# Performance work log

Measured on AMD Instinct MI355X. Metric: run time of the kernel, lower is better.

Reference implementation:

```python
import jax, jax.numpy as jnp
from jax import lax
import numpy as np

EPS_DENOM = 1e-5
EPS_NCC = 1e-5
HIGH = 0.5  # IntensityNormalization(high=0.5): min-max rescale of weights to [0, high]


def _box_conv(v, kernel):
    # Dense ones-kernel 3D box filter, VALID padding, stride 1 (NCDHW / OIDHW).
    return lax.conv_general_dilated(
        v, kernel, window_strides=(1, 1, 1), padding='VALID',
        dimension_numbers=('NCDHW', 'OIDHW', 'NCDHW'))


def setup_inputs() -> dict:
    key = jax.random.key(0)
    k1, k2 = jax.random.split(key)
    shape = (2, 1, 160, 192, 160)
    y_pred = jax.random.normal(k1, shape, dtype=jnp.float32)
    y_true = jax.random.normal(k2, shape, dtype=jnp.float32)
    kernel = jnp.ones((1, 1, 7, 7, 7), dtype=jnp.float32)
    return {"y_pred": y_pred, "y_true": y_true, "kernel": kernel}


def reference(y_pred, y_true, kernel):
    nw = kernel.sum()  # = 343 for a 7^3 ones kernel
    x, y = y_pred, y_true
    sum_x = _box_conv(x, kernel)
    sum_y = _box_conv(y, kernel)
    sum_x2 = _box_conv(x * x, kernel)
    sum_y2 = _box_conv(y * y, kernel)
    sum_xy = _box_conv(x * y, kernel)

    mean_x = sum_x / nw
    mean_y = sum_y / nw
    num = sum_xy + mean_x * mean_y * nw - mean_x * sum_y - mean_y * sum_x
    denom_0 = mean_x * mean_x * nw + sum_x2 - 2.0 * mean_x * sum_x
    denom_1 = mean_y * mean_y * nw + sum_y2 - 2.0 * mean_y * sum_y
    denom = denom_0 * denom_1

    valid = denom > EPS_DENOM
    safe_denom = jnp.where(valid, denom, 1.0)
    ncc = jnp.where(valid, num / jnp.sqrt(safe_denom), 0.0)
    invalid = (ncc < -1.0 - EPS_NCC) | (ncc > 1.0 + EPS_NCC)
    ncc = jnp.where(invalid, 0.0, ncc)
    all_valid = valid & ~invalid

    # Intensity normalization of weights: min-max rescale of local variance sum
    # over the valid voxels to [0, HIGH], then normalize to sum to 1.
    v = 0.5 * (denom_0 + denom_1)
    vmin = jnp.min(jnp.where(all_valid, v, jnp.inf))
    vmax = jnp.max(jnp.where(all_valid, v, -jnp.inf))
    w = jnp.where(all_valid, (v - vmin) / (vmax - vmin + 1e-12) * HIGH, 0.0)
    w = w / w.sum()

    return 1.0 - jnp.sum(jnp.where(all_valid, ncc, 0.0) * w)
```

## Files before the change

### kernel.cpp

```cpp
#include <hip/hip_runtime.h>
#include <math.h>

#define NN 2
#define DD 160
#define HH 192
#define WW 160
#define DO 154
#define HO 186
#define WO 154

#define NWO 3
#define HOT 8
#define NHO 24
#define ZCH 8
#define ZOC 20
#define NB (NWO * NHO * NN * ZCH)

#define LDS_SYNC() do { __builtin_amdgcn_s_waitcnt(0xC07F); __builtin_amdgcn_s_barrier(); } while (0)

__device__ __forceinline__ float block_sum(float v, float* sm) {
  int tid = threadIdx.x;
  sm[tid] = v;
  __syncthreads();
#pragma unroll
  for (int off = 128; off > 0; off >>= 1) {
    if (tid < off) sm[tid] += sm[tid + off];
    __syncthreads();
  }
  float r = sm[0];
  __syncthreads();
  return r;
}

__device__ __forceinline__ float block_min(float v, float* sm) {
  int tid = threadIdx.x;
  sm[tid] = v;
  __syncthreads();
#pragma unroll
  for (int off = 128; off > 0; off >>= 1) {
    if (tid < off) sm[tid] = fminf(sm[tid], sm[tid + off]);
    __syncthreads();
  }
  float r = sm[0];
  __syncthreads();
  return r;
}

__device__ __forceinline__ float wave_sum(float v) {
  v += __shfl_xor(v, 32); v += __shfl_xor(v, 16); v += __shfl_xor(v, 8);
  v += __shfl_xor(v, 4);  v += __shfl_xor(v, 2);  v += __shfl_xor(v, 1);
  return v;
}

__device__ __forceinline__ float wave_min(float v) {
  v = fminf(v, __shfl_xor(v, 32)); v = fminf(v, __shfl_xor(v, 16));
  v = fminf(v, __shfl_xor(v, 8));  v = fminf(v, __shfl_xor(v, 4));
  v = fminf(v, __shfl_xor(v, 2));  v = fminf(v, __shfl_xor(v, 1));
  return v;
}

#define SLIDE7(V, M) do { \
  float s0 = ((V[0]+V[1])+(V[2]+V[3])) + ((V[4]+V[5])+V[6]); \
  float s1 = s0 - V[0] + V[7]; \
  float s2 = s1 - V[1] + V[8]; \
  float s3 = s2 - V[2] + V[9]; \
  float s4 = s3 - V[3] + V[10]; \
  float s5 = s4 - V[4] + V[11]; \
  float s6 = s5 - V[5] + V[12]; \
  float s7 = s6 - V[6] + V[13]; \
  *(float4*)&R[M][0][rA][c4] = make_float4(s0, s1, s2, s3); \
  *(float4*)&R[M][1][rA][c4] = make_float4(s4, s5, s6, s7); \
} while (0)

__global__ __launch_bounds__(256, 3) void ncc_fused(const float* __restrict__ X,
                                                    const float* __restrict__ Y,
                                                    float* __restrict__ part) {
  __shared__ __align__(16) float R[5][2][14][64];
  __shared__ __align__(16) float Mh[5][HOT][64];
  __shared__ float red[4][5];

  const int tid = threadIdx.x;
  const int tx = tid & 63, ty = tid >> 6;
  const int wo0 = blockIdx.x * 64;
  const int ho0 = blockIdx.y * HOT;
  const int n   = blockIdx.z >> 3;
  const int ck  = blockIdx.z & 7;
  const int z0  = ck * ZOC;
  const int zout = min(ZOC, DO - z0);
  const int nslice = zout + 6;

  const int wo = wo0 + tx;
  const bool act0 = (wo < WO) && (ho0 + ty < HO);
  const bool act1 = (wo < WO) && (ho0 + ty + 4 < HO);

  const size_t slice = (size_t)HH * WW;
  const float* Xn = X + (size_t)n * DD * slice;
  const float* Yn = Y + (size_t)n * DD * slice;
  const float inv_nw = 1.0f / 343.0f;
  const float LO = -1.0f - 1e-5f, HI = 1.0f + 1e-5f;

  const int pA  = tid;
  const bool hasA = (pA < 112);
  const int rA  = pA >> 3;
  const int c8  = (pA & 7) << 3;
  const int c4  = (pA & 7) << 2;
  const int hA  = ho0 + rA;
  const int baseW = wo0 + c8;
  const bool okA  = hasA && (hA < HH) && (baseW < WO);
  const bool tail = okA && (baseW + 14 > WW);
  const float* XrowA = Xn + (size_t)hA * WW + baseW;
  const float* YrowA = Yn + (size_t)hA * WW + baseW;

  float4 lx0={0,0,0,0}, lx1={0,0,0,0}, lx2={0,0,0,0};
  float4 ly0={0,0,0,0}, ly1={0,0,0,0}, ly2={0,0,0,0};
  float2 lx3={0,0}, ly3={0,0};

  auto loadA = [&](int s_in) {
    if (okA) {
      const float* xp = XrowA + (size_t)(z0 + s_in) * slice;
      const float* yp = YrowA + (size_t)(z0 + s_in) * slice;
      lx0 = *(const float4*)xp;       lx1 = *(const float4*)(xp + 4);
      ly0 = *(const float4*)yp;       ly1 = *(const float4*)(yp + 4);
      if (!tail) {
        lx2 = *(const float4*)(xp + 8); lx3 = *(const float2*)(xp + 12);
        ly2 = *(const float4*)(yp + 8); ly3 = *(const float2*)(yp + 12);
      } else {
        lx2 = make_float4(0.f,0.f,0.f,0.f); lx3 = make_float2(0.f,0.f);
        ly2 = make_float4(0.f,0.f,0.f,0.f); ly3 = make_float2(0.f,0.f);
      }
    }
  };

  auto storeA = [&]() {
    if (okA) {
      const float x[14] = {lx0.x,lx0.y,lx0.z,lx0.w, lx1.x,lx1.y,lx1.z,lx1.w,
                           lx2.x,lx2.y,lx2.z,lx2.w, lx3.x,lx3.y};
      const float y[14] = {ly0.x,ly0.y,ly0.z,ly0.w, ly1.x,ly1.y,ly1.z,ly1.w,
                           ly2.x,ly2.y,ly2.z,ly2.w, ly3.x,ly3.y};
      SLIDE7(x, 0);
      SLIDE7(y, 1);
      {
        float t[14];
#pragma unroll
        for (int i = 0; i < 14; ++i) t[i] = x[i] * x[i];
        SLIDE7(t, 2);
      }
      {
        float t[14];
#pragma unroll
        for (int i = 0; i < 14; ++i) t[i] = y[i] * y[i];
        SLIDE7(t, 3);
      }
      {
        float t[14];
#pragma unroll
        for (int i = 0; i < 14; ++i) t[i] = x[i] * y[i];
        SLIDE7(t, 4);
      }
    }
  };

  auto phaseHitem = [&](int ch, int w) {
    const int q = w >> 3, j = w & 7;
    const float* rp = &R[ch][j >> 2][0][(q << 2) + (j & 3)];
    float r0=rp[0],   r1=rp[64],  r2=rp[128], r3=rp[192], r4=rp[256],
          r5=rp[320], r6=rp[384], r7=rp[448], r8=rp[512], r9=rp[576],
          r10=rp[640], r11=rp[704], r12=rp[768], r13=rp[832];
    float m0 = ((r0+r1)+(r2+r3)) + ((r4+r5)+r6);
    float m1 = m0 - r0 + r7;
    float m2 = m1 - r1 + r8;
    float m3 = m2 - r2 + r9;
    float m4 = m3 - r3 + r10;
    float m5 = m4 - r4 + r11;
    float m6 = m5 - r5 + r12;
    float m7 = m6 - r6 + r13;
    Mh[ch][0][w]=m0; Mh[ch][1][w]=m1; Mh[ch][2][w]=m2; Mh[ch][3][w]=m3;
    Mh[ch][4][w]=m4; Mh[ch][5][w]=m5; Mh[ch][6][w]=m6; Mh[ch][7][w]=m7;
  };
  auto phaseH = [&]() {
    phaseHitem(ty, tx);
    if (tid < 64) phaseHitem(4, tid);
  };

  float zs0[2]={0,0}, zs1[2]={0,0}, zs2[2]={0,0}, zs3[2]={0,0}, zs4[2]={0,0};
  float h0[2][7], h1[2][7], h2[2][7], h3[2][7], h4[2][7];
#pragma unroll
  for (int j = 0; j < 7; ++j) {
    h0[0][j]=0.f; h1[0][j]=0.f; h2[0][j]=0.f; h3[0][j]=0.f; h4[0][j]=0.f;
    h0[1][j]=0.f; h1[1][j]=0.f; h2[1][j]=0.f; h3[1][j]=0.f; h4[1][j]=0.f;
  }
  float p_snv = 0.f, p_sn = 0.f, p_sv = 0.f, p_cnt = 0.f, p_vmin = 3.4e38f;

  loadA(0);
  storeA();
  __syncthreads();

  for (int sb = 0; sb < nslice; sb += 7) {
#pragma unroll
    for (int u = 0; u < 7; ++u) {
      const int s = sb + u;
      if (s < nslice) {
        if (s + 1 < nslice) loadA(s + 1);
        phaseH();
        LDS_SYNC();
        {
#pragma unroll
          for (int rb = 0; rb < 2; ++rb) {
            const int row = ty + (rb << 2);
            float m0 = Mh[0][row][tx], m1 = Mh[1][row][tx], m2 = Mh[2][row][tx],
                  m3 = Mh[3][row][tx], m4 = Mh[4][row][tx];
            zs0[rb] += m0 - h0[rb][u]; h0[rb][u] = m0;
            zs1[rb] += m1 - h1[rb][u]; h1[rb][u] = m1;
            zs2[rb] += m2 - h2[rb][u]; h2[rb][u] = m2;
            zs3[rb] += m3 - h3[rb][u]; h3[rb][u] = m3;
            zs4[rb] += m4 - h4[rb][u]; h4[rb][u] = m4;
            if (s >= 6 && (rb ? act1 : act0)) {
              float num = zs4[rb] - zs0[rb] * zs1[rb] * inv_nw;
              float d0  = zs2[rb] - zs0[rb] * zs0[rb] * inv_nw;
              float d1  = zs3[rb] - zs1[rb] * zs1[rb] * inv_nw;
              float den = d0 * d1;
              if (den > 1e-5f) {
                float ncc = num * __frsqrt_rn(den);
                if (ncc >= LO && ncc <= HI) {
                  float v = 0.5f * (d0 + d1);
                  p_snv += ncc * v; p_sn += ncc; p_sv += v; p_cnt += 1.f;
                  p_vmin = fminf(p_vmin, v);
                }
              }
            }
          }
        }
        if (s + 1 < nslice) storeA();
        LDS_SYNC();
      }
    }
  }

  float r0 = wave_sum(p_snv);
  float r1 = wave_sum(p_sn);
  float r2 = wave_sum(p_sv);
  float r3 = wave_sum(p_cnt);
  float r4 = wave_min(p_vmin);
  if (tx == 0) {
    red[ty][0]=r0; red[ty][1]=r1; red[ty][2]=r2; red[ty][3]=r3; red[ty][4]=r4;
  }
  __syncthreads();
  if (tid == 0) {
    float s0 = (red[0][0]+red[1][0]) + (red[2][0]+red[3][0]);
    float s1 = (red[0][1]+red[1][1]) + (red[2][1]+red[3][1]);
    float s2 = (red[0][2]+red[1][2]) + (red[2][2]+red[3][2]);
    float s3 = (red[0][3]+red[1][3]) + (red[2][3]+red[3][3]);
    float s4 = fminf(fminf(red[0][4],red[1][4]), fminf(red[2][4],red[3][4]));
    const int bid = blockIdx.x + NWO * (blockIdx.y + NHO * blockIdx.z);
    float* pp = part + (size_t)bid * 8;
    pp[0] = s0; pp[1] = s1; pp[2] = s2; pp[3] = s3; pp[4] = s4;
  }
}

__global__ __launch_bounds__(256) void fin(const float* __restrict__ part,
                                           float* __restrict__ out) {
  __shared__ float sm[256];
  const int tid = threadIdx.x;
  float s0 = 0.f, s1 = 0.f, s2 = 0.f, s3 = 0.f, vm = 3.4e38f;
  for (int b = tid; b < NB; b += 256) {
    const float* pp = part + (size_t)b * 8;
    s0 += pp[0]; s1 += pp[1]; s2 += pp[2]; s3 += pp[3];
    vm = fminf(vm, pp[4]);
  }
  s0 = block_sum(s0, sm);
  s1 = block_sum(s1, sm);
  s2 = block_sum(s2, sm);
  s3 = block_sum(s3, sm);
  vm = block_min(vm, sm);
  if (tid == 0) {
    out[0] = 1.0f - (s0 - vm * s1) / (s2 - vm * s3);
  }
}

extern "C" void kernel_launch(void* const* d_in, const int* in_sizes, int n_in,
                              void* d_out, int out_size, void* d_ws, size_t ws_size,
                              hipStream_t stream) {
  const float* X = (const float*)d_in[0];
  const float* Y = (const float*)d_in[1];

  float* part = (float*)d_ws;

  dim3 g(NWO, NHO, NN * ZCH);
  ncc_fused<<<g, 256, 0, stream>>>(X, Y, part);
  fin<<<1, 256, 0, stream>>>(part, (float*)d_out);
}
```

Measured before the change: 164.8 us.

## Halve per-thread W-pass width, raise occupancy and rebalance Z chunking

The W-direction sliding sum now has each thread produce 4 outputs from 10 loaded values instead of 8 from 14, using 224 loader threads instead of 112. The R staging buffer loses its split dimension, which halves its LDS footprint and simplifies the H-pass indexing. Launch bounds go from 3 to 4 blocks per SM and the Z split changes from 8 chunks of 20 to 7 chunks of 22. The aim is better occupancy and more load parallelism, at the cost of more redundant halo loads and more register pressure per wave.

```diff
diff --git a/kernel.cpp b/kernel.cpp
--- a/kernel.cpp
+++ b/kernel.cpp
@@ -12,8 +12,8 @@
 #define NWO 3
 #define HOT 8
 #define NHO 24
-#define ZCH 8
-#define ZOC 20
+#define ZCH 7
+#define ZOC 22
 #define NB (NWO * NHO * NN * ZCH)
 
 #define LDS_SYNC() do { __builtin_amdgcn_s_waitcnt(0xC07F); __builtin_amdgcn_s_barrier(); } while (0)
@@ -64,18 +64,13 @@
   float s1 = s0 - V[0] + V[7]; \
   float s2 = s1 - V[1] + V[8]; \
   float s3 = s2 - V[2] + V[9]; \
-  float s4 = s3 - V[3] + V[10]; \
-  float s5 = s4 - V[4] + V[11]; \
-  float s6 = s5 - V[5] + V[12]; \
-  float s7 = s6 - V[6] + V[13]; \
-  *(float4*)&R[M][0][rA][c4] = make_float4(s0, s1, s2, s3); \
-  *(float4*)&R[M][1][rA][c4] = make_float4(s4, s5, s6, s7); \
+  *(float4*)&R[M][rA][c4] = make_float4(s0, s1, s2, s3); \
 } while (0)
 
-__global__ __launch_bounds__(256, 3) void ncc_fused(const float* __restrict__ X,
+__global__ __launch_bounds__(256, 4) void ncc_fused(const float* __restrict__ X,
                                                     const float* __restrict__ Y,
                                                     float* __restrict__ part) {
-  __shared__ __align__(16) float R[5][2][14][64];
+  __shared__ __align__(16) float R[5][14][64];
   __shared__ __align__(16) float Mh[5][HOT][64];
   __shared__ float red[4][5];
 
@@ -83,8 +78,8 @@
   const int tx = tid & 63, ty = tid >> 6;
   const int wo0 = blockIdx.x * 64;
   const int ho0 = blockIdx.y * HOT;
-  const int n   = blockIdx.z >> 3;
-  const int ck  = blockIdx.z & 7;
+  const int n   = blockIdx.z / ZCH;
+  const int ck  = blockIdx.z % ZCH;
   const int z0  = ck * ZOC;
   const int zout = min(ZOC, DO - z0);
   const int nslice = zout + 6;
@@ -100,20 +95,19 @@
   const float LO = -1.0f - 1e-5f, HI = 1.0f + 1e-5f;
 
   const int pA  = tid;
-  const bool hasA = (pA < 112);
-  const int rA  = pA >> 3;
-  const int c8  = (pA & 7) << 3;
-  const int c4  = (pA & 7) << 2;
+  const bool hasA = (pA < 224);
+  const int rA  = pA >> 4;
+  const int c4  = (pA & 15) << 2;
   const int hA  = ho0 + rA;
-  const int baseW = wo0 + c8;
+  const int baseW = wo0 + c4;
   const bool okA  = hasA && (hA < HH) && (baseW < WO);
-  const bool tail = okA && (baseW + 14 > WW);
+  const bool tail = okA && (baseW + 10 > WW);
   const float* XrowA = Xn + (size_t)hA * WW + baseW;
   const float* YrowA = Yn + (size_t)hA * WW + baseW;
 
-  float4 lx0={0,0,0,0}, lx1={0,0,0,0}, lx2={0,0,0,0};
-  float4 ly0={0,0,0,0}, ly1={0,0,0,0}, ly2={0,0,0,0};
-  float2 lx3={0,0}, ly3={0,0};
+  float4 lx0={0,0,0,0}, lx1={0,0,0,0};
+  float4 ly0={0,0,0,0}, ly1={0,0,0,0};
+  float2 lx2={0,0}, ly2={0,0};
 
   auto loadA = [&](int s_in) {
     if (okA) {
@@ -121,48 +115,40 @@
       const float* yp = YrowA + (size_t)(z0 + s_in) * slice;
       lx0 = *(const float4*)xp;       lx1 = *(const float4*)(xp + 4);
       ly0 = *(const float4*)yp;       ly1 = *(const float4*)(yp + 4);
-      if (!tail) {
-        lx2 = *(const float4*)(xp + 8); lx3 = *(const float2*)(xp + 12);
-        ly2 = *(const float4*)(yp + 8); ly3 = *(const float2*)(yp + 12);
-      } else {
-        lx2 = make_float4(0.f,0.f,0.f,0.f); lx3 = make_float2(0.f,0.f);
-        ly2 = make_float4(0.f,0.f,0.f,0.f); ly3 = make_float2(0.f,0.f);
-      }
+      if (!tail) { lx2 = *(const float2*)(xp + 8); ly2 = *(const float2*)(yp + 8); }
+      else       { lx2 = make_float2(0.f, 0.f);    ly2 = make_float2(0.f, 0.f); }
     }
   };
 
   auto storeA = [&]() {
     if (okA) {
-      const float x[14] = {lx0.x,lx0.y,lx0.z,lx0.w, lx1.x,lx1.y,lx1.z,lx1.w,
-                           lx2.x,lx2.y,lx2.z,lx2.w, lx3.x,lx3.y};
-      const float y[14] = {ly0.x,ly0.y,ly0.z,ly0.w, ly1.x,ly1.y,ly1.z,ly1.w,
-                           ly2.x,ly2.y,ly2.z,ly2.w, ly3.x,ly3.y};
+      const float x[10] = {lx0.x,lx0.y,lx0.z,lx0.w, lx1.x,lx1.y,lx1.z,lx1.w, lx2.x,lx2.y};
+      const float y[10] = {ly0.x,ly0.y,ly0.z,ly0.w, ly1.x,ly1.y,ly1.z,ly1.w, ly2.x,ly2.y};
       SLIDE7(x, 0);
       SLIDE7(y, 1);
       {
-        float t[14];
-#pragma unroll
-        for (int i = 0; i < 14; ++i) t[i] = x[i] * x[i];
+        float t[10];
+#pragma unroll
+        for (int i = 0; i < 10; ++i) t[i] = x[i] * x[i];
         SLIDE7(t, 2);
       }
       {
-        float t[14];
-#pragma unroll
-        for (int i = 0; i < 14; ++i) t[i] = y[i] * y[i];
+        float t[10];
+#pragma unroll
+        for (int i = 0; i < 10; ++i) t[i] = y[i] * y[i];
         SLIDE7(t, 3);
       }
       {
-        float t[14];
-#pragma unroll
-        for (int i = 0; i < 14; ++i) t[i] = x[i] * y[i];
+        float t[10];
+#pragma unroll
+        for (int i = 0; i < 10; ++i) t[i] = x[i] * y[i];
         SLIDE7(t, 4);
       }
     }
   };
 
   auto phaseHitem = [&](int ch, int w) {
-    const int q = w >> 3, j = w & 7;
-    const float* rp = &R[ch][j >> 2][0][(q << 2) + (j & 3)];
+    const float* rp = &R[ch][0][w];
     float r0=rp[0],   r1=rp[64],  r2=rp[128], r3=rp[192], r4=rp[256],
           r5=rp[320], r6=rp[384], r7=rp[448], r8=rp[512], r9=rp[576],
           r10=rp[640], r11=rp[704], r12=rp[768], r13=rp[832];
@@ -179,7 +165,7 @@
   };
   auto phaseH = [&]() {
     phaseHitem(ty, tx);
-    if (tid < 64) phaseHitem(4, tid);
+    if (ty == 3) phaseHitem(4, tx);
   };
 
   float zs0[2]={0,0}, zs1[2]={0,0}, zs2[2]={0,0}, zs3[2]={0,0}, zs4[2]={0,0};
```

After: 168.5 us. +2.3%, slower.

## Use 512-thread blocks with one output row per wave and fixed z-chunks

Applied to the files above, without the earlier changes.

Doubles the block to 512 threads so each wave owns a single output row instead of two. The H-direction sliding sum is split so 320 threads each handle one (channel, column) pair, and the R buffer drops its split-half layout. Z is partitioned into 7 chunks of 22 outputs with a constant slice count, which removes the per-block tail checks and allows the outer loop to be left unrolled. This trades fewer registers and more parallelism per block against lower occupancy per SIMD and some idle threads during each phase.

```diff
diff --git a/kernel.cpp b/kernel.cpp
--- a/kernel.cpp
+++ b/kernel.cpp
@@ -12,8 +12,9 @@
 #define NWO 3
 #define HOT 8
 #define NHO 24
-#define ZCH 8
-#define ZOC 20
+#define ZCH 7
+#define ZOC 22
+#define NSL 28
 #define NB (NWO * NHO * NN * ZCH)
 
 #define LDS_SYNC() do { __builtin_amdgcn_s_waitcnt(0xC07F); __builtin_amdgcn_s_barrier(); } while (0)
@@ -59,7 +60,7 @@
   return v;
 }
 
-#define SLIDE7(V, M) do { \
+#define SLIDE7W8(V, M) do { \
   float s0 = ((V[0]+V[1])+(V[2]+V[3])) + ((V[4]+V[5])+V[6]); \
   float s1 = s0 - V[0] + V[7]; \
   float s2 = s1 - V[1] + V[8]; \
@@ -68,30 +69,27 @@
   float s5 = s4 - V[4] + V[11]; \
   float s6 = s5 - V[5] + V[12]; \
   float s7 = s6 - V[6] + V[13]; \
-  *(float4*)&R[M][0][rA][c4] = make_float4(s0, s1, s2, s3); \
-  *(float4*)&R[M][1][rA][c4] = make_float4(s4, s5, s6, s7); \
+  *(float4*)&R[M][rA][c8]     = make_float4(s0, s1, s2, s3); \
+  *(float4*)&R[M][rA][c8 + 4] = make_float4(s4, s5, s6, s7); \
 } while (0)
 
-__global__ __launch_bounds__(256, 3) void ncc_fused(const float* __restrict__ X,
+__global__ __launch_bounds__(512, 2) void ncc_fused(const float* __restrict__ X,
                                                     const float* __restrict__ Y,
                                                     float* __restrict__ part) {
-  __shared__ __align__(16) float R[5][2][14][64];
+  __shared__ __align__(16) float R[5][14][64];
   __shared__ __align__(16) float Mh[5][HOT][64];
-  __shared__ float red[4][5];
+  __shared__ float red[8][5];
 
   const int tid = threadIdx.x;
-  const int tx = tid & 63, ty = tid >> 6;
+  const int tx = tid & 63, wv = tid >> 6;
   const int wo0 = blockIdx.x * 64;
   const int ho0 = blockIdx.y * HOT;
-  const int n   = blockIdx.z >> 3;
-  const int ck  = blockIdx.z & 7;
+  const int n   = blockIdx.z / ZCH;
+  const int ck  = blockIdx.z % ZCH;
   const int z0  = ck * ZOC;
-  const int zout = min(ZOC, DO - z0);
-  const int nslice = zout + 6;
 
   const int wo = wo0 + tx;
-  const bool act0 = (wo < WO) && (ho0 + ty < HO);
-  const bool act1 = (wo < WO) && (ho0 + ty + 4 < HO);
+  const bool act = (wo < WO) && (ho0 + wv < HO);
 
   const size_t slice = (size_t)HH * WW;
   const float* Xn = X + (size_t)n * DD * slice;
@@ -103,7 +101,6 @@
   const bool hasA = (pA < 112);
   const int rA  = pA >> 3;
   const int c8  = (pA & 7) << 3;
-  const int c4  = (pA & 7) << 2;
   const int hA  = ho0 + rA;
   const int baseW = wo0 + c8;
   const bool okA  = hasA && (hA < HH) && (baseW < WO);
@@ -137,102 +134,95 @@
                            lx2.x,lx2.y,lx2.z,lx2.w, lx3.x,lx3.y};
       const float y[14] = {ly0.x,ly0.y,ly0.z,ly0.w, ly1.x,ly1.y,ly1.z,ly1.w,
                            ly2.x,ly2.y,ly2.z,ly2.w, ly3.x,ly3.y};
-      SLIDE7(x, 0);
-      SLIDE7(y, 1);
+      SLIDE7W8(x, 0);
+      SLIDE7W8(y, 1);
       {
         float t[14];
 #pragma unroll
         for (int i = 0; i < 14; ++i) t[i] = x[i] * x[i];
-        SLIDE7(t, 2);
+        SLIDE7W8(t, 2);
       }
       {
         float t[14];
 #pragma unroll
         for (int i = 0; i < 14; ++i) t[i] = y[i] * y[i];
-        SLIDE7(t, 3);
+        SLIDE7W8(t, 3);
       }
       {
         float t[14];
 #pragma unroll
         for (int i = 0; i < 14; ++i) t[i] = x[i] * y[i];
-        SLIDE7(t, 4);
+        SLIDE7W8(t, 4);
       }
     }
   };
 
-  auto phaseHitem = [&](int ch, int w) {
-    const int q = w >> 3, j = w & 7;
-    const float* rp = &R[ch][j >> 2][0][(q << 2) + (j & 3)];
-    float r0=rp[0],   r1=rp[64],  r2=rp[128], r3=rp[192], r4=rp[256],
-          r5=rp[320], r6=rp[384], r7=rp[448], r8=rp[512], r9=rp[576],
-          r10=rp[640], r11=rp[704], r12=rp[768], r13=rp[832];
-    float m0 = ((r0+r1)+(r2+r3)) + ((r4+r5)+r6);
-    float m1 = m0 - r0 + r7;
-    float m2 = m1 - r1 + r8;
-    float m3 = m2 - r2 + r9;
-    float m4 = m3 - r3 + r10;
-    float m5 = m4 - r4 + r11;
-    float m6 = m5 - r5 + r12;
-    float m7 = m6 - r6 + r13;
-    Mh[ch][0][w]=m0; Mh[ch][1][w]=m1; Mh[ch][2][w]=m2; Mh[ch][3][w]=m3;
-    Mh[ch][4][w]=m4; Mh[ch][5][w]=m5; Mh[ch][6][w]=m6; Mh[ch][7][w]=m7;
+  const int idxH = tid - 128;
+  const bool okH = (tid >= 128) && (idxH < 320);
+  const int chH = okH ? (idxH >> 6) : 0;
+  const int wH  = idxH & 63;
+  const float* rpH = &R[chH][0][wH];
+
+  auto phaseH = [&]() {
+    if (okH) {
+      float w0 = rpH[0],   w1 = rpH[64],  w2 = rpH[128], w3 = rpH[192],
+            w4 = rpH[256], w5 = rpH[320], w6 = rpH[384];
+      float m = ((w0+w1)+(w2+w3)) + ((w4+w5)+w6);
+      Mh[chH][0][wH] = m;
+      float nw;
+      nw = rpH[448]; m = m - w0 + nw; Mh[chH][1][wH] = m;
+      nw = rpH[512]; m = m - w1 + nw; Mh[chH][2][wH] = m;
+      nw = rpH[576]; m = m - w2 + nw; Mh[chH][3][wH] = m;
+      nw = rpH[640]; m = m - w3 + nw; Mh[chH][4][wH] = m;
+      nw = rpH[704]; m = m - w4 + nw; Mh[chH][5][wH] = m;
+      nw = rpH[768]; m = m - w5 + nw; Mh[chH][6][wH] = m;
+      nw = rpH[832]; m = m - w6 + nw; Mh[chH][7][wH] = m;
+    }
   };
-  auto phaseH = [&]() {
-    phaseHitem(ty, tx);
-    if (tid < 64) phaseHitem(4, tid);
-  };
-
-  float zs0[2]={0,0}, zs1[2]={0,0}, zs2[2]={0,0}, zs3[2]={0,0}, zs4[2]={0,0};
-  float h0[2][7], h1[2][7], h2[2][7], h3[2][7], h4[2][7];
-#pragma unroll
-  for (int j = 0; j < 7; ++j) {
-    h0[0][j]=0.f; h1[0][j]=0.f; h2[0][j]=0.f; h3[0][j]=0.f; h4[0][j]=0.f;
-    h0[1][j]=0.f; h1[1][j]=0.f; h2[1][j]=0.f; h3[1][j]=0.f; h4[1][j]=0.f;
-  }
+
+  float zs0=0.f, zs1=0.f, zs2=0.f, zs3=0.f, zs4=0.f;
+  float h0[7], h1[7], h2[7], h3[7], h4[7];
+#pragma unroll
+  for (int j = 0; j < 7; ++j) { h0[j]=0.f; h1[j]=0.f; h2[j]=0.f; h3[j]=0.f; h4[j]=0.f; }
   float p_snv = 0.f, p_sn = 0.f, p_sv = 0.f, p_cnt = 0.f, p_vmin = 3.4e38f;
 
   loadA(0);
   storeA();
   __syncthreads();
 
-  for (int sb = 0; sb < nslice; sb += 7) {
+#pragma unroll 1
+  for (int sb = 0; sb < NSL; sb += 7) {
 #pragma unroll
     for (int u = 0; u < 7; ++u) {
       const int s = sb + u;
-      if (s < nslice) {
-        if (s + 1 < nslice) loadA(s + 1);
-        phaseH();
-        LDS_SYNC();
-        {
-#pragma unroll
-          for (int rb = 0; rb < 2; ++rb) {
-            const int row = ty + (rb << 2);
-            float m0 = Mh[0][row][tx], m1 = Mh[1][row][tx], m2 = Mh[2][row][tx],
-                  m3 = Mh[3][row][tx], m4 = Mh[4][row][tx];
-            zs0[rb] += m0 - h0[rb][u]; h0[rb][u] = m0;
-            zs1[rb] += m1 - h1[rb][u]; h1[rb][u] = m1;
-            zs2[rb] += m2 - h2[rb][u]; h2[rb][u] = m2;
-            zs3[rb] += m3 - h3[rb][u]; h3[rb][u] = m3;
-            zs4[rb] += m4 - h4[rb][u]; h4[rb][u] = m4;
-            if (s >= 6 && (rb ? act1 : act0)) {
-              float num = zs4[rb] - zs0[rb] * zs1[rb] * inv_nw;
-              float d0  = zs2[rb] - zs0[rb] * zs0[rb] * inv_nw;
-              float d1  = zs3[rb] - zs1[rb] * zs1[rb] * inv_nw;
-              float den = d0 * d1;
-              if (den > 1e-5f) {
-                float ncc = num * __frsqrt_rn(den);
-                if (ncc >= LO && ncc <= HI) {
-                  float v = 0.5f * (d0 + d1);
-                  p_snv += ncc * v; p_sn += ncc; p_sv += v; p_cnt += 1.f;
-                  p_vmin = fminf(p_vmin, v);
-                }
-              }
+      if (s + 1 < NSL) loadA(s + 1);
+      phaseH();
+      LDS_SYNC();
+      {
+        float m0 = Mh[0][wv][tx], m1 = Mh[1][wv][tx], m2 = Mh[2][wv][tx],
+              m3 = Mh[3][wv][tx], m4 = Mh[4][wv][tx];
+        zs0 += m0 - h0[u]; h0[u] = m0;
+        zs1 += m1 - h1[u]; h1[u] = m1;
+        zs2 += m2 - h2[u]; h2[u] = m2;
+        zs3 += m3 - h3[u]; h3[u] = m3;
+        zs4 += m4 - h4[u]; h4[u] = m4;
+        if (s >= 6 && act) {
+          float num = zs4 - zs0 * zs1 * inv_nw;
+          float d0  = zs2 - zs0 * zs0 * inv_nw;
+          float d1  = zs3 - zs1 * zs1 * inv_nw;
+          float den = d0 * d1;
+          if (den > 1e-5f) {
+            float ncc = num * __frsqrt_rn(den);
+            if (ncc >= LO && ncc <= HI) {
+              float v = 0.5f * (d0 + d1);
+              p_snv += ncc * v; p_sn += ncc; p_sv += v; p_cnt += 1.f;
+              p_vmin = fminf(p_vmin, v);
             }
           }
         }
-        if (s + 1 < nslice) storeA();
-        LDS_SYNC();
-      }
+      }
+      if (s + 1 < NSL) storeA();
+      LDS_SYNC();
     }
   }
 
@@ -242,15 +232,16 @@
   float r3 = wave_sum(p_cnt);
   float r4 = wave_min(p_vmin);
   if (tx == 0) {
-    red[ty][0]=r0; red[ty][1]=r1; red[ty][2]=r2; red[ty][3]=r3; red[ty][4]=r4;
+    red[wv][0]=r0; red[wv][1]=r1; red[wv][2]=r2; red[wv][3]=r3; red[wv][4]=r4;
   }
   __syncthreads();
   if (tid == 0) {
-    float s0 = (red[0][0]+red[1][0]) + (red[2][0]+red[3][0]);
-    float s1 = (red[0][1]+red[1][1]) + (red[2][1]+red[3][1]);
-    float s2 = (red[0][2]+red[1][2]) + (red[2][2]+red[3][2]);
-    float s3 = (red[0][3]+red[1][3]) + (red[2][3]+red[3][3]);
-    float s4 = fminf(fminf(red[0][4],red[1][4]), fminf(red[2][4],red[3][4]));
+    float s0=0.f, s1=0.f, s2=0.f, s3=0.f, s4=3.4e38f;
+#pragma unroll
+    for (int w = 0; w < 8; ++w) {
+      s0 += red[w][0]; s1 += red[w][1]; s2 += red[w][2]; s3 += red[w][3];
+      s4 = fminf(s4, red[w][4]);
+    }
     const int bid = blockIdx.x + NWO * (blockIdx.y + NHO * blockIdx.z);
     float* pp = part + (size_t)bid * 8;
     pp[0] = s0; pp[1] = s1; pp[2] = s2; pp[3] = s3; pp[4] = s4;
@@ -286,6 +277,6 @@
   float* part = (float*)d_ws;
 
   dim3 g(NWO, NHO, NN * ZCH);
-  ncc_fused<<<g, 256, 0, stream>>>(X, Y, part);
+  ncc_fused<<<g, 512, 0, stream>>>(X, Y, part);
   fin<<<1, 256, 0, stream>>>(part, (float*)d_out);
 }
```

Result: no change. 166.5 us (+1.1%).
